# Performance work log

Hardware: AMD Instinct MI355X
Metric: run time of the kernel (lower is better)

## Reference

```python
import math
import jax, jax.numpy as jnp
import numpy as np

B, C, HH, WW = 1, 256, 64, 64
NUM_HEADS = 8
GROUPS = 8
EPS = 1e-5


def setup_inputs() -> dict:
    key = jax.random.key(0)
    ks = jax.random.split(key, 5)
    x = jax.random.normal(ks[0], (B, C, HH, WW), dtype=jnp.float32)
    gn_gamma = jnp.ones((C,), dtype=jnp.float32)
    gn_beta = jnp.zeros((C,), dtype=jnp.float32)
    qkv_w = jax.random.normal(ks[1], (3 * C, C), dtype=jnp.float32) / math.sqrt(C)
    qkv_b = jax.random.normal(ks[2], (3 * C,), dtype=jnp.float32) * 0.02
    proj_w = jax.random.normal(ks[3], (C, C), dtype=jnp.float32) / math.sqrt(C)
    proj_b = jax.random.normal(ks[4], (C,), dtype=jnp.float32) * 0.02
    return {"x": x, "gn_gamma": gn_gamma, "gn_beta": gn_beta,
            "qkv_w": qkv_w, "qkv_b": qkv_b, "proj_w": proj_w, "proj_b": proj_b}


def reference(x, gn_gamma, gn_beta, qkv_w, qkv_b, proj_w, proj_b):
    b, c, h, w = x.shape
    t = h * w
    xf = x.reshape(b, c, t)
    # GroupNorm(8, C): normalize over (C/8 channels x T spatial) per group
    xg = xf.reshape(b, GROUPS, (c // GROUPS) * t)
    mean = xg.mean(axis=-1, keepdims=True)
    var = xg.var(axis=-1, keepdims=True)
    xn = ((xg - mean) * jax.lax.rsqrt(var + EPS)).reshape(b, c, t)
    xn = xn * gn_gamma[:, None] + gn_beta[:, None]
    # 1x1 Conv1d C -> 3C is a channel matmul
    qkv = jnp.einsum('oc,bct->bot', qkv_w, xn) + qkv_b[:, None]  # [b, 3C, t]
    nh = NUM_HEADS
    ch = c // nh
    q, k, v = jnp.split(qkv, 3, axis=1)  # each [b, C, t]
    q = q.reshape(b * nh, ch, t)
    k = k.reshape(b * nh, ch, t)
    v = v.reshape(b * nh, ch, t)
    scale = 1.0 / math.sqrt(math.sqrt(ch))
    weight = jnp.einsum('bct,bcs->bts', q * scale, k * scale)  # [b*nh, t, t]
    weight = jax.nn.softmax(weight.astype(jnp.float32), axis=-1).astype(qkv.dtype)
    a = jnp.einsum('bts,bcs->bct', weight, v).reshape(b, c, t)
    hout = jnp.einsum('oc,bct->bot', proj_w, a) + proj_b[:, None]
    return x + hout.reshape(b, c, h, w)
```

## Files before the change

kernel.cpp:

```cpp
#include <hip/hip_runtime.h>
#include <hip/hip_bf16.h>
#include <math.h>

#define C_DIM 256
#define T_DIM 4096
#define NHEADS 8
#define NGROUPS 8
#define NSPLIT 4
#define SRANGE (T_DIM / NSPLIT)
#define NT (SRANGE / 64)

typedef __attribute__((ext_vector_type(8))) short bf16x8;
typedef __attribute__((ext_vector_type(4))) float f32x4;

#if __has_builtin(__builtin_amdgcn_exp2f)
#define EXP2(x) __builtin_amdgcn_exp2f(x)
#else
#define EXP2(x) exp2f(x)
#endif

#define MFMA16(a, b, c) __builtin_amdgcn_mfma_f32_16x16x32_bf16(a, b, c, 0, 0, 0)

#define WS_PSUM 0
#define WS_PSQ  256
#define WS_QT_F   1024
#define WS_KT_F   (WS_QT_F + 524288)
#define WS_VB_F   (WS_KT_F + 524288)
#define WS_WQB_F  (WS_VB_F + 524288)
#define WS_WPB_F  (WS_WQB_F + 98304)
#define WS_OP_F   (WS_WPB_F + 32768)
#define WS_L_F    (WS_OP_F + NSPLIT * T_DIM * 256 / 2)

#define QSCALE 0.2550348527f

__device__ __forceinline__ ushort f2bf(float f) {
  union { float f; unsigned u; } v; v.f = f;
  return (ushort)((v.u + 0x7fffu + ((v.u >> 16) & 1u)) >> 16);
}

__device__ __forceinline__ float bf2f(ushort u) {
  union { unsigned u; float f; } v; v.u = ((unsigned)u) << 16;
  return v.f;
}

__device__ __forceinline__ uint pk2(float a, float b) {
  __hip_bfloat162 h = __float22bfloat162_rn(make_float2(a, b));
  union { __hip_bfloat162 h; uint u; } c; c.h = h; return c.u;
}

__global__ __launch_bounds__(256) void prep(const float* __restrict__ x,
                                            const float* __restrict__ wq,
                                            const float* __restrict__ wp,
                                            float* __restrict__ ws,
                                            ushort* __restrict__ wqb,
                                            ushort* __restrict__ wpb) {
  const int i4 = (blockIdx.x * 256 + threadIdx.x) * 4;
  const int n1 = 768 * 256;
  if (i4 < n1) {
    float4 v = *(const float4*)(wq + i4);
    union { ushort us[4]; uint2 u; } pk;
    pk.us[0] = f2bf(v.x); pk.us[1] = f2bf(v.y); pk.us[2] = f2bf(v.z); pk.us[3] = f2bf(v.w);
    *(uint2*)(wqb + i4) = pk.u;
  } else {
    const int j = i4 - n1;
    float4 v = *(const float4*)(wp + j);
    union { ushort us[4]; uint2 u; } pk;
    pk.us[0] = f2bf(v.x); pk.us[1] = f2bf(v.y); pk.us[2] = f2bf(v.z); pk.us[3] = f2bf(v.w);
    *(uint2*)(wpb + j) = pk.u;
  }
  const int g = blockIdx.x >> 5;
  const int bx = blockIdx.x & 31;
  const size_t base = (size_t)g * 131072 + (size_t)bx * 4096;
  float s = 0.f, s2 = 0.f;
  for (int i = threadIdx.x; i < 4096; i += 256) {
    float v = x[base + i];
    s += v;
    s2 += v * v;
  }
#pragma unroll
  for (int mask = 1; mask <= 32; mask <<= 1) {
    s += __shfl_xor(s, mask, 64);
    s2 += __shfl_xor(s2, mask, 64);
  }
  __shared__ float red[8];
  const int wid = threadIdx.x >> 6;
  if ((threadIdx.x & 63) == 0) { red[wid] = s; red[4 + wid] = s2; }
  __syncthreads();
  if (threadIdx.x == 0) {
    ws[WS_PSUM + g * 32 + bx] = red[0] + red[1] + red[2] + red[3];
    ws[WS_PSQ + g * 32 + bx] = red[4] + red[5] + red[6] + red[7];
  }
}

__global__ __launch_bounds__(256) void qkv_mfma(const float* __restrict__ x,
                                                const float* __restrict__ gamma,
                                                const float* __restrict__ beta,
                                                const float* __restrict__ ws,
                                                const ushort* __restrict__ wqb,
                                                const float* __restrict__ bias,
                                                ushort* __restrict__ qt,
                                                ushort* __restrict__ kt,
                                                ushort* __restrict__ vb) {
  const int t0 = blockIdx.x * 16;
  const int oc = blockIdx.y;
  __shared__ ushort A[16 * 256];
  __shared__ float fg[256], fb[256];
  __shared__ float sm_stat[16];
  const int tid = threadIdx.x;
  {
    const int gg = tid >> 5, i = tid & 31;
    float s = ws[WS_PSUM + gg * 32 + i];
    float s2 = ws[WS_PSQ + gg * 32 + i];
#pragma unroll
    for (int mask = 1; mask <= 16; mask <<= 1) {
      s += __shfl_xor(s, mask, 32);
      s2 += __shfl_xor(s2, mask, 32);
    }
    if (i == 0) {
      const float inv_n = 1.0f / 131072.0f;
      float mean = s * inv_n;
      float var = s2 * inv_n - mean * mean;
      sm_stat[gg] = mean;
      sm_stat[8 + gg] = rsqrtf(var + 1e-5f);
    }
  }
  __syncthreads();
  {
    const int c = tid, gg = c >> 5;
    float fgv = gamma[c] * sm_stat[8 + gg];
    fg[c] = fgv; fb[c] = beta[c] - sm_stat[gg] * fgv;
  }
  __syncthreads();
#pragma unroll
  for (int p = 0; p < 4; ++p) {
    const int idx = p * 256 + tid;
    const int c = idx >> 2;
    const int tin = (idx & 3) * 4;
    float4 xv = *(const float4*)(x + (size_t)c * T_DIM + t0 + tin);
    const float fgc = fg[c], fbc = fb[c];
    float xn[4] = {fmaf(xv.x, fgc, fbc), fmaf(xv.y, fgc, fbc),
                   fmaf(xv.z, fgc, fbc), fmaf(xv.w, fgc, fbc)};
#pragma unroll
    for (int i = 0; i < 4; ++i) {
      const int t = tin + i;
      A[t * 256 + (c ^ ((t & 7) << 3))] = f2bf(xn[i]);
    }
  }
  __syncthreads();

  const int w = tid >> 6, lane = tid & 63, l15 = lane & 15, g = lane >> 4;
  const int o_loc = w * 64;
  f32x4 acc[4] = {};
  const ushort* wrow[4];
#pragma unroll
  for (int j = 0; j < 4; ++j)
    wrow[j] = wqb + (size_t)(oc * 256 + o_loc + j * 16 + l15) * 256;

  bf16x8 bc[4], bn[4];
#pragma unroll
  for (int j = 0; j < 4; ++j) bc[j] = *(const bf16x8*)(wrow[j] + 8 * g);

#pragma unroll
  for (int kk = 0; kk < 8; ++kk) {
    const bf16x8 af = *(const bf16x8*)(&A[l15 * 256 + ((kk * 32 + 8 * g) ^ ((l15 & 7) << 3))]);
    if (kk < 7) {
#pragma unroll
      for (int j = 0; j < 4; ++j) bn[j] = *(const bf16x8*)(wrow[j] + (kk + 1) * 32 + 8 * g);
    }
#pragma unroll
    for (int j = 0; j < 4; ++j)
      acc[j] = MFMA16(af, bc[j], acc[j]);
#pragma unroll
    for (int j = 0; j < 4; ++j) bc[j] = bn[j];
  }

  if (oc == 2) {
#pragma unroll
    for (int j = 0; j < 4; ++j) {
      const int o = o_loc + j * 16 + l15;
      const float bo = bias[512 + o];
      union { ushort us[4]; uint2 u; } pk;
#pragma unroll
      for (int r = 0; r < 4; ++r) pk.us[r] = f2bf(acc[j][r] + bo);
      *(uint2*)(vb + (size_t)o * T_DIM + t0 + 4 * g) = pk.u;
    }
  } else {
    const float scale = (oc == 0) ? QSCALE : 1.0f;
    __syncthreads();
#pragma unroll
    for (int j = 0; j < 4; ++j) {
      const int o = o_loc + j * 16 + l15;
      const float bo = bias[oc * 256 + o];
#pragma unroll
      for (int r = 0; r < 4; ++r) {
        const int t = 4 * g + r;
        A[t * 256 + (o ^ ((t & 7) << 3))] = f2bf((acc[j][r] + bo) * scale);
      }
    }
    __syncthreads();
    ushort* dst = (oc == 0) ? qt : kt;
    const int hh = tid >> 5;
    const int tt = (tid >> 1) & 15;
    const int d0 = (tid & 1) * 16;
    const int sw = (tt & 7) << 3;
    uint4 v0 = *(uint4*)&A[tt * 256 + ((hh * 32 + d0) ^ sw)];
    uint4 v1 = *(uint4*)&A[tt * 256 + ((hh * 32 + d0 + 8) ^ sw)];
    ushort* gp = dst + ((size_t)hh * T_DIM + t0 + tt) * 32 + d0;
    *(uint4*)gp = v0;
    *(uint4*)(gp + 8) = v1;
  }
}

__global__ __launch_bounds__(256, 4) void attn_fwd(const ushort* __restrict__ qt,
                                                   const ushort* __restrict__ kt,
                                                   const ushort* __restrict__ vb,
                                                   ushort* __restrict__ Op,
                                                   float* __restrict__ Lb) {
  const int bid = blockIdx.x;
  const int h = bid & 7;
  const int inner = bid >> 3;
  const int qb = inner & 31;
  const int z = inner >> 5;
  const int tid = threadIdx.x;
  const int w = tid >> 6, lane = tid & 63, l15 = lane & 15, g = lane >> 4;

  __shared__ ushort Klds[2][64 * 40];
  __shared__ ushort Vlds[2][32 * 72];

  const int t_a = qb * 128 + w * 16 + l15;
  const int t_b = t_a + 64;
  const bf16x8 qfa = *(const bf16x8*)(qt + ((size_t)(h * T_DIM + t_a) * 32 + 8 * g));
  const bf16x8 qfb = *(const bf16x8*)(qt + ((size_t)(h * T_DIM + t_b) * 32 + 8 * g));

  f32x4 Oa0 = {}, Oa1 = {}, Ob0 = {}, Ob1 = {};
  float la = 0.f, lb = 0.f;

  const int sbeg = z * SRANGE;
  const int p_row = tid >> 2;
  const int q5 = p_row & 31;
  const int sm_row = (p_row & 32) + 16 * ((q5 >> 2) & 1) + 4 * (q5 >> 3) + (q5 & 3);
  const ushort* kgp = kt + (size_t)h * T_DIM * 32 + (size_t)(sbeg + p_row) * 32 + (tid & 3) * 8;
  const ushort* vgp = vb + (size_t)(h * 32 + (tid >> 3)) * T_DIM + sbeg + (tid & 7) * 8;
  ushort* kw0 = &Klds[0][sm_row * 40 + (tid & 3) * 8];
  ushort* vw0 = &Vlds[0][(tid >> 3) * 72 + (tid & 7) * 8];
  {
    *(uint4*)kw0 = *(const uint4*)kgp;
    *(uint4*)vw0 = *(const uint4*)vgp;
  }
  uint4 kn = *(const uint4*)(kgp + 2048);
  uint4 vn = *(const uint4*)(vgp + 64);
  __syncthreads();

  int cur = 0;
  for (int t = 0; t < NT; ++t) {
    if (t + 1 < NT) {
      *(uint4*)(kw0 + (cur ^ 1) * (64 * 40)) = kn;
      *(uint4*)(vw0 + (cur ^ 1) * (32 * 72)) = vn;
      if (t + 2 < NT) {
        kn = *(const uint4*)(kgp + (size_t)(t + 2) * 2048);
        vn = *(const uint4*)(vgp + (t + 2) * 64);
      }
    }

    const ushort* kbase = &Klds[cur][0];
    const ushort* vbase = &Vlds[cur][0];
    const f32x4 z4 = {};
    const bf16x8 kf0 = *(const bf16x8*)(kbase + (0 * 16 + l15) * 40 + 8 * g);
    const bf16x8 kf1 = *(const bf16x8*)(kbase + (1 * 16 + l15) * 40 + 8 * g);
    const bf16x8 kf2 = *(const bf16x8*)(kbase + (2 * 16 + l15) * 40 + 8 * g);
    const bf16x8 kf3 = *(const bf16x8*)(kbase + (3 * 16 + l15) * 40 + 8 * g);
    __builtin_amdgcn_s_setprio(1);
    f32x4 sa0 = MFMA16(kf0, qfa, z4);
    f32x4 sa1 = MFMA16(kf1, qfa, z4);
    f32x4 sa2 = MFMA16(kf2, qfa, z4);
    f32x4 sa3 = MFMA16(kf3, qfa, z4);
    f32x4 sb0 = MFMA16(kf0, qfb, z4);
    f32x4 sb1 = MFMA16(kf1, qfb, z4);
    f32x4 sb2 = MFMA16(kf2, qfb, z4);
    f32x4 sb3 = MFMA16(kf3, qfb, z4);
    __builtin_amdgcn_s_setprio(0);

    const bf16x8 vf00 = *(const bf16x8*)(vbase + (l15) * 72 + 8 * g);
    const bf16x8 vf01 = *(const bf16x8*)(vbase + (l15) * 72 + 32 + 8 * g);
    const bf16x8 vf10 = *(const bf16x8*)(vbase + (16 + l15) * 72 + 8 * g);
    const bf16x8 vf11 = *(const bf16x8*)(vbase + (16 + l15) * 72 + 32 + 8 * g);

    union { uint u[4]; bf16x8 v; } fa0, fa1, fb0, fb1;
    {
      float p0, p1, p2, p3, p4, p5, p6, p7;
      p0 = EXP2(sa0[0]); p1 = EXP2(sa0[1]); p2 = EXP2(sa0[2]); p3 = EXP2(sa0[3]);
      p4 = EXP2(sa1[0]); p5 = EXP2(sa1[1]); p6 = EXP2(sa1[2]); p7 = EXP2(sa1[3]);
      la += ((p0 + p1) + (p2 + p3)) + ((p4 + p5) + (p6 + p7));
      fa0.u[0] = pk2(p0, p1); fa0.u[1] = pk2(p2, p3);
      fa0.u[2] = pk2(p4, p5); fa0.u[3] = pk2(p6, p7);
      p0 = EXP2(sa2[0]); p1 = EXP2(sa2[1]); p2 = EXP2(sa2[2]); p3 = EXP2(sa2[3]);
      p4 = EXP2(sa3[0]); p5 = EXP2(sa3[1]); p6 = EXP2(sa3[2]); p7 = EXP2(sa3[3]);
      la += ((p0 + p1) + (p2 + p3)) + ((p4 + p5) + (p6 + p7));
      fa1.u[0] = pk2(p0, p1); fa1.u[1] = pk2(p2, p3);
      fa1.u[2] = pk2(p4, p5); fa1.u[3] = pk2(p6, p7);
    }

    __builtin_amdgcn_s_setprio(1);
    Oa0 = MFMA16(vf00, fa0.v, Oa0);
    Oa0 = MFMA16(vf01, fa1.v, Oa0);
    Oa1 = MFMA16(vf10, fa0.v, Oa1);
    Oa1 = MFMA16(vf11, fa1.v, Oa1);
    __builtin_amdgcn_s_setprio(0);

    {
      float p0, p1, p2, p3, p4, p5, p6, p7;
      p0 = EXP2(sb0[0]); p1 = EXP2(sb0[1]); p2 = EXP2(sb0[2]); p3 = EXP2(sb0[3]);
      p4 = EXP2(sb1[0]); p5 = EXP2(sb1[1]); p6 = EXP2(sb1[2]); p7 = EXP2(sb1[3]);
      lb += ((p0 + p1) + (p2 + p3)) + ((p4 + p5) + (p6 + p7));
      fb0.u[0] = pk2(p0, p1); fb0.u[1] = pk2(p2, p3);
      fb0.u[2] = pk2(p4, p5); fb0.u[3] = pk2(p6, p7);
      p0 = EXP2(sb2[0]); p1 = EXP2(sb2[1]); p2 = EXP2(sb2[2]); p3 = EXP2(sb2[3]);
      p4 = EXP2(sb3[0]); p5 = EXP2(sb3[1]); p6 = EXP2(sb3[2]); p7 = EXP2(sb3[3]);
      lb += ((p0 + p1) + (p2 + p3)) + ((p4 + p5) + (p6 + p7));
      fb1.u[0] = pk2(p0, p1); fb1.u[1] = pk2(p2, p3);
      fb1.u[2] = pk2(p4, p5); fb1.u[3] = pk2(p6, p7);
    }

    __builtin_amdgcn_s_setprio(1);
    Ob0 = MFMA16(vf00, fb0.v, Ob0);
    Ob0 = MFMA16(vf01, fb1.v, Ob0);
    Ob1 = MFMA16(vf10, fb0.v, Ob1);
    Ob1 = MFMA16(vf11, fb1.v, Ob1);
    __builtin_amdgcn_s_setprio(0);

    __syncthreads();
    cur ^= 1;
  }

  ushort* opz = Op + (size_t)z * T_DIM * 256;
  {
    union { ushort us[4]; uint2 u; } p0, p1;
#pragma unroll
    for (int r = 0; r < 4; ++r) { p0.us[r] = f2bf(Oa0[r]); p1.us[r] = f2bf(Oa1[r]); }
    *(uint2*)(opz + (size_t)t_a * 256 + h * 32 + 4 * g) = p0.u;
    *(uint2*)(opz + (size_t)t_a * 256 + h * 32 + 16 + 4 * g) = p1.u;
#pragma unroll
    for (int r = 0; r < 4; ++r) { p0.us[r] = f2bf(Ob0[r]); p1.us[r] = f2bf(Ob1[r]); }
    *(uint2*)(opz + (size_t)t_b * 256 + h * 32 + 4 * g) = p0.u;
    *(uint2*)(opz + (size_t)t_b * 256 + h * 32 + 16 + 4 * g) = p1.u;
  }
  la += __shfl_xor(la, 16, 64);
  la += __shfl_xor(la, 32, 64);
  lb += __shfl_xor(lb, 16, 64);
  lb += __shfl_xor(lb, 32, 64);
  if (g == 0) {
    Lb[(size_t)(z * NHEADS + h) * T_DIM + t_a] = la;
    Lb[(size_t)(z * NHEADS + h) * T_DIM + t_b] = lb;
  }
}

__global__ __launch_bounds__(256) void proj_mfma(const ushort* __restrict__ Op,
                                                 const float* __restrict__ Lb,
                                                 const ushort* __restrict__ wpb,
                                                 const float* __restrict__ bias,
                                                 const float* __restrict__ x,
                                                 float* __restrict__ out) {
  const int t0 = blockIdx.x * 16;
  __shared__ ushort A[16 * 256];
  __shared__ float rinv[128];
  const int tid = threadIdx.x;
  if (tid < 128) {
    const int h = tid >> 4, tt = tid & 15;
    float l = 0.f;
#pragma unroll
    for (int zz = 0; zz < NSPLIT; ++zz)
      l += Lb[(size_t)(zz * NHEADS + h) * T_DIM + t0 + tt];
    rinv[tid] = 1.0f / l;
  }
  __syncthreads();
#pragma unroll
  for (int p = 0; p < 2; ++p) {
    const int t = p * 8 + (tid >> 5);
    const int c0 = (tid & 31) * 8;
    float a8[8] = {0.f, 0.f, 0.f, 0.f, 0.f, 0.f, 0.f, 0.f};
#pragma unroll
    for (int zz = 0; zz < NSPLIT; ++zz) {
      uint4 v = *(const uint4*)(Op + ((size_t)zz * T_DIM + t0 + t) * 256 + c0);
      const ushort* us = (const ushort*)&v;
#pragma unroll
      for (int i = 0; i < 8; ++i) a8[i] += bf2f(us[i]);
    }
    const float ri = rinv[(c0 >> 5) * 16 + t];
    union { ushort us[8]; uint4 u; } pk;
#pragma unroll
    for (int i = 0; i < 8; ++i) pk.us[i] = f2bf(a8[i] * ri);
    *(uint4*)&A[t * 256 + (c0 ^ ((t & 7) << 3))] = pk.u;
  }
  __syncthreads();

  const int w = tid >> 6, lane = tid & 63, l15 = lane & 15, g = lane >> 4;
  const int o0 = w * 64;
  f32x4 acc[4] = {};
  const ushort* wrow[4];
#pragma unroll
  for (int j = 0; j < 4; ++j)
    wrow[j] = wpb + (size_t)(o0 + 16 * j + l15) * 256;

#pragma unroll
  for (int kk = 0; kk < 8; ++kk) {
    const bf16x8 af = *(const bf16x8*)(&A[l15 * 256 + ((kk * 32 + 8 * g) ^ ((l15 & 7) << 3))]);
#pragma unroll
    for (int j = 0; j < 4; ++j) {
      const bf16x8 bfr = *(const bf16x8*)(wrow[j] + kk * 32 + 8 * g);
      acc[j] = MFMA16(af, bfr, acc[j]);
    }
  }

#pragma unroll
  for (int j = 0; j < 4; ++j) {
    const int o = o0 + 16 * j + l15;
    const float bo = bias[o];
    const size_t base = (size_t)o * T_DIM + t0 + 4 * g;
    const float4 xr = *(const float4*)(x + base);
    float4 ov;
    ov.x = acc[j][0] + bo + xr.x;
    ov.y = acc[j][1] + bo + xr.y;
    ov.z = acc[j][2] + bo + xr.z;
    ov.w = acc[j][3] + bo + xr.w;
    *(float4*)(out + base) = ov;
  }
}

extern "C" void kernel_launch(void* const* d_in, const int* in_sizes, int n_in,
                              void* d_out, int out_size, void* d_ws, size_t ws_size,
                              hipStream_t stream) {
  const float* x      = (const float*)d_in[0];
  const float* gamma  = (const float*)d_in[1];
  const float* beta   = (const float*)d_in[2];
  const float* qkv_w  = (const float*)d_in[3];
  const float* qkv_b  = (const float*)d_in[4];
  const float* proj_w = (const float*)d_in[5];
  const float* proj_b = (const float*)d_in[6];
  float* out = (float*)d_out;
  float* ws  = (float*)d_ws;

  ushort* qt  = (ushort*)(ws + WS_QT_F);
  ushort* kt  = (ushort*)(ws + WS_KT_F);
  ushort* vb  = (ushort*)(ws + WS_VB_F);
  ushort* wqb = (ushort*)(ws + WS_WQB_F);
  ushort* wpb = (ushort*)(ws + WS_WPB_F);
  ushort* Op  = (ushort*)(ws + WS_OP_F);
  float*  Lb  = ws + WS_L_F;

  prep<<<256, 256, 0, stream>>>(x, qkv_w, proj_w, ws, wqb, wpb);
  qkv_mfma<<<dim3(256, 3), 256, 0, stream>>>(x, gamma, beta, ws, wqb, qkv_b, qt, kt, vb);
  attn_fwd<<<NHEADS * 32 * NSPLIT, 256, 0, stream>>>(qt, kt, vb, Op, Lb);
  proj_mfma<<<256, 256, 0, stream>>>(Op, Lb, wpb, proj_b, x, out);
}
```

Before: 66.57 us.

## Process two K/V tiles per barrier with four-slot LDS double buffering

New measurement: 117.0 us. 75.8% more time.

```diff
diff --git a/kernel.cpp b/kernel.cpp
--- a/kernel.cpp
+++ b/kernel.cpp
@@ -224,8 +224,8 @@
   const int tid = threadIdx.x;
   const int w = tid >> 6, lane = tid & 63, l15 = lane & 15, g = lane >> 4;
 
-  __shared__ ushort Klds[2][64 * 40];
-  __shared__ ushort Vlds[2][32 * 72];
+  __shared__ ushort Klds[4][64 * 40];
+  __shared__ ushort Vlds[4][32 * 72];
 
   const int t_a = qb * 128 + w * 16 + l15;
   const int t_b = t_a + 64;
@@ -243,27 +243,18 @@
   const ushort* vgp = vb + (size_t)(h * 32 + (tid >> 3)) * T_DIM + sbeg + (tid & 7) * 8;
   ushort* kw0 = &Klds[0][sm_row * 40 + (tid & 3) * 8];
   ushort* vw0 = &Vlds[0][(tid >> 3) * 72 + (tid & 7) * 8];
-  {
-    *(uint4*)kw0 = *(const uint4*)kgp;
-    *(uint4*)vw0 = *(const uint4*)vgp;
-  }
-  uint4 kn = *(const uint4*)(kgp + 2048);
-  uint4 vn = *(const uint4*)(vgp + 64);
-  __syncthreads();
-
-  int cur = 0;
-  for (int t = 0; t < NT; ++t) {
-    if (t + 1 < NT) {
-      *(uint4*)(kw0 + (cur ^ 1) * (64 * 40)) = kn;
-      *(uint4*)(vw0 + (cur ^ 1) * (32 * 72)) = vn;
-      if (t + 2 < NT) {
-        kn = *(const uint4*)(kgp + (size_t)(t + 2) * 2048);
-        vn = *(const uint4*)(vgp + (t + 2) * 64);
-      }
-    }
-
-    const ushort* kbase = &Klds[cur][0];
-    const ushort* vbase = &Vlds[cur][0];
+
+  *(uint4*)kw0 = *(const uint4*)kgp;
+  *(uint4*)(kw0 + 2560) = *(const uint4*)(kgp + 2048);
+  *(uint4*)vw0 = *(const uint4*)vgp;
+  *(uint4*)(vw0 + 2304) = *(const uint4*)(vgp + 64);
+  uint4 kn0 = *(const uint4*)(kgp + 2 * 2048);
+  uint4 kn1 = *(const uint4*)(kgp + 3 * 2048);
+  uint4 vn0 = *(const uint4*)(vgp + 2 * 64);
+  uint4 vn1 = *(const uint4*)(vgp + 3 * 64);
+  __syncthreads();
+
+  auto tile_body = [&](const ushort* kbase, const ushort* vbase) {
     const f32x4 z4 = {};
     const bf16x8 kf0 = *(const bf16x8*)(kbase + (0 * 16 + l15) * 40 + 8 * g);
     const bf16x8 kf1 = *(const bf16x8*)(kbase + (1 * 16 + l15) * 40 + 8 * g);
@@ -327,6 +318,26 @@
     Ob1 = MFMA16(vf10, fb0.v, Ob1);
     Ob1 = MFMA16(vf11, fb1.v, Ob1);
     __builtin_amdgcn_s_setprio(0);
+  };
+
+  int cur = 0;
+  for (int t = 0; t < NT; t += 2) {
+    if (t + 2 < NT) {
+      const int dst = (cur ^ 1) * 2;
+      *(uint4*)(kw0 + dst * 2560) = kn0;
+      *(uint4*)(kw0 + (dst + 1) * 2560) = kn1;
+      *(uint4*)(vw0 + dst * 2304) = vn0;
+      *(uint4*)(vw0 + (dst + 1) * 2304) = vn1;
+      if (t + 4 < NT) {
+        kn0 = *(const uint4*)(kgp + (size_t)(t + 4) * 2048);
+        kn1 = *(const uint4*)(kgp + (size_t)(t + 5) * 2048);
+        vn0 = *(const uint4*)(vgp + (t + 4) * 64);
+        vn1 = *(const uint4*)(vgp + (t + 5) * 64);
+      }
+    }
+
+    tile_body(&Klds[cur * 2][0], &Vlds[cur * 2][0]);
+    tile_body(&Klds[cur * 2 + 1][0], &Vlds[cur * 2 + 1][0]);
 
     __syncthreads();
     cur ^= 1;
```

## Load K/V MFMA fragments directly from global memory, drop LDS staging

Applied to the files above, without the earlier changes.

After: 118.1 us. +77.4%, slower.

```diff
diff --git a/kernel.cpp b/kernel.cpp
--- a/kernel.cpp
+++ b/kernel.cpp
@@ -222,10 +222,8 @@
   const int qb = inner & 31;
   const int z = inner >> 5;
   const int tid = threadIdx.x;
-  const int w = tid >> 6, lane = tid & 63, l15 = lane & 15, g = lane >> 4;
-
-  __shared__ ushort Klds[2][64 * 40];
-  __shared__ ushort Vlds[2][32 * 72];
+  const int lane = tid & 63, l15 = lane & 15, g = lane >> 4;
+  const int w = tid >> 6;
 
   const int t_a = qb * 128 + w * 16 + l15;
   const int t_b = t_a + 64;
@@ -236,54 +234,52 @@
   float la = 0.f, lb = 0.f;
 
   const int sbeg = z * SRANGE;
-  const int p_row = tid >> 2;
-  const int q5 = p_row & 31;
-  const int sm_row = (p_row & 32) + 16 * ((q5 >> 2) & 1) + 4 * (q5 >> 3) + (q5 & 3);
-  const ushort* kgp = kt + (size_t)h * T_DIM * 32 + (size_t)(sbeg + p_row) * 32 + (tid & 3) * 8;
-  const ushort* vgp = vb + (size_t)(h * 32 + (tid >> 3)) * T_DIM + sbeg + (tid & 7) * 8;
-  ushort* kw0 = &Klds[0][sm_row * 40 + (tid & 3) * 8];
-  ushort* vw0 = &Vlds[0][(tid >> 3) * 72 + (tid & 7) * 8];
-  {
-    *(uint4*)kw0 = *(const uint4*)kgp;
-    *(uint4*)vw0 = *(const uint4*)vgp;
-  }
-  uint4 kn = *(const uint4*)(kgp + 2048);
-  uint4 vn = *(const uint4*)(vgp + 64);
-  __syncthreads();
-
-  int cur = 0;
-  for (int t = 0; t < NT; ++t) {
-    if (t + 1 < NT) {
-      *(uint4*)(kw0 + (cur ^ 1) * (64 * 40)) = kn;
-      *(uint4*)(vw0 + (cur ^ 1) * (32 * 72)) = vn;
-      if (t + 2 < NT) {
-        kn = *(const uint4*)(kgp + (size_t)(t + 2) * 2048);
-        vn = *(const uint4*)(vgp + (t + 2) * 64);
-      }
-    }
-
-    const ushort* kbase = &Klds[cur][0];
-    const ushort* vbase = &Vlds[cur][0];
+  const int send = sbeg + SRANGE;
+  const ushort* kb = kt + (size_t)h * T_DIM * 32;
+  const ushort* vbs = vb + (size_t)h * 32 * T_DIM;
+
+  int koff[4];
+#pragma unroll
+  for (int so = 0; so < 4; ++so) {
+    const int sm = so * 16 + l15;
+    koff[so] = (32 * (sm >> 5) + 8 * ((sm >> 2) & 3) + 4 * ((sm >> 4) & 1) + (sm & 3)) * 32 + 8 * g;
+  }
+  const int voff0 = l15 * T_DIM + 8 * g;
+  const int voff1 = l15 * T_DIM + 32 + 8 * g;
+  const int voff2 = (16 + l15) * T_DIM + 8 * g;
+  const int voff3 = (16 + l15) * T_DIM + 32 + 8 * g;
+
+  bf16x8 kf[4], vf[4];
+#pragma unroll
+  for (int so = 0; so < 4; ++so)
+    kf[so] = *(const bf16x8*)(kb + (size_t)sbeg * 32 + koff[so]);
+  vf[0] = *(const bf16x8*)(vbs + sbeg + voff0);
+  vf[1] = *(const bf16x8*)(vbs + sbeg + voff1);
+  vf[2] = *(const bf16x8*)(vbs + sbeg + voff2);
+  vf[3] = *(const bf16x8*)(vbs + sbeg + voff3);
+
+  for (int s0 = sbeg; s0 < send; s0 += 64) {
+    const int sn = (s0 + 64 < send) ? s0 + 64 : sbeg;
+    bf16x8 nkf[4], nvf[4];
+#pragma unroll
+    for (int so = 0; so < 4; ++so)
+      nkf[so] = *(const bf16x8*)(kb + (size_t)sn * 32 + koff[so]);
+    nvf[0] = *(const bf16x8*)(vbs + sn + voff0);
+    nvf[1] = *(const bf16x8*)(vbs + sn + voff1);
+    nvf[2] = *(const bf16x8*)(vbs + sn + voff2);
+    nvf[3] = *(const bf16x8*)(vbs + sn + voff3);
+
     const f32x4 z4 = {};
-    const bf16x8 kf0 = *(const bf16x8*)(kbase + (0 * 16 + l15) * 40 + 8 * g);
-    const bf16x8 kf1 = *(const bf16x8*)(kbase + (1 * 16 + l15) * 40 + 8 * g);
-    const bf16x8 kf2 = *(const bf16x8*)(kbase + (2 * 16 + l15) * 40 + 8 * g);
-    const bf16x8 kf3 = *(const bf16x8*)(kbase + (3 * 16 + l15) * 40 + 8 * g);
     __builtin_amdgcn_s_setprio(1);
-    f32x4 sa0 = MFMA16(kf0, qfa, z4);
-    f32x4 sa1 = MFMA16(kf1, qfa, z4);
-    f32x4 sa2 = MFMA16(kf2, qfa, z4);
-    f32x4 sa3 = MFMA16(kf3, qfa, z4);
-    f32x4 sb0 = MFMA16(kf0, qfb, z4);
-    f32x4 sb1 = MFMA16(kf1, qfb, z4);
-    f32x4 sb2 = MFMA16(kf2, qfb, z4);
-    f32x4 sb3 = MFMA16(kf3, qfb, z4);
+    f32x4 sa0 = MFMA16(kf[0], qfa, z4);
+    f32x4 sa1 = MFMA16(kf[1], qfa, z4);
+    f32x4 sa2 = MFMA16(kf[2], qfa, z4);
+    f32x4 sa3 = MFMA16(kf[3], qfa, z4);
+    f32x4 sb0 = MFMA16(kf[0], qfb, z4);
+    f32x4 sb1 = MFMA16(kf[1], qfb, z4);
+    f32x4 sb2 = MFMA16(kf[2], qfb, z4);
+    f32x4 sb3 = MFMA16(kf[3], qfb, z4);
     __builtin_amdgcn_s_setprio(0);
-
-    const bf16x8 vf00 = *(const bf16x8*)(vbase + (l15) * 72 + 8 * g);
-    const bf16x8 vf01 = *(const bf16x8*)(vbase + (l15) * 72 + 32 + 8 * g);
-    const bf16x8 vf10 = *(const bf16x8*)(vbase + (16 + l15) * 72 + 8 * g);
-    const bf16x8 vf11 = *(const bf16x8*)(vbase + (16 + l15) * 72 + 32 + 8 * g);
 
     union { uint u[4]; bf16x8 v; } fa0, fa1, fb0, fb1;
     {
@@ -301,10 +297,10 @@
     }
 
     __builtin_amdgcn_s_setprio(1);
-    Oa0 = MFMA16(vf00, fa0.v, Oa0);
-    Oa0 = MFMA16(vf01, fa1.v, Oa0);
-    Oa1 = MFMA16(vf10, fa0.v, Oa1);
-    Oa1 = MFMA16(vf11, fa1.v, Oa1);
+    Oa0 = MFMA16(vf[0], fa0.v, Oa0);
+    Oa0 = MFMA16(vf[1], fa1.v, Oa0);
+    Oa1 = MFMA16(vf[2], fa0.v, Oa1);
+    Oa1 = MFMA16(vf[3], fa1.v, Oa1);
     __builtin_amdgcn_s_setprio(0);
 
     {
@@ -322,14 +318,16 @@
     }
 
     __builtin_amdgcn_s_setprio(1);
-    Ob0 = MFMA16(vf00, fb0.v, Ob0);
-    Ob0 = MFMA16(vf01, fb1.v, Ob0);
-    Ob1 = MFMA16(vf10, fb0.v, Ob1);
-    Ob1 = MFMA16(vf11, fb1.v, Ob1);
+    Ob0 = MFMA16(vf[0], fb0.v, Ob0);
+    Ob0 = MFMA16(vf[1], fb1.v, Ob0);
+    Ob1 = MFMA16(vf[2], fb0.v, Ob1);
+    Ob1 = MFMA16(vf[3], fb1.v, Ob1);
     __builtin_amdgcn_s_setprio(0);
 
-    __syncthreads();
-    cur ^= 1;
+#pragma unroll
+    for (int so = 0; so < 4; ++so) kf[so] = nkf[so];
+#pragma unroll
+    for (int u = 0; u < 4; ++u) vf[u] = nvf[u];
   }
 
   ushort* opz = Op + (size_t)z * T_DIM * 256;
```
